# Optimization experiments

Hardware: AMD Instinct MI355X
Metric: run time of the kernel (lower is better)

The kernel has to match this reference:

```python
import jax, jax.numpy as jnp
import numpy as np

HID = 512
EMB = 768
TOP_K = 8
LN_EPS = 1e-5
NORM_EPS = 1e-12


def _mlp_ln(x, W1, b1, W2, b2, g, beta):
    # Linear -> ReLU -> Linear -> LayerNorm
    h = jax.nn.relu(x @ W1 + b1)
    h = h @ W2 + b2
    mu = jnp.mean(h, axis=-1, keepdims=True)
    var = jnp.var(h, axis=-1, keepdims=True)
    return (h - mu) * jax.lax.rsqrt(var + LN_EPS) * g + beta


def _l2norm(x):
    n = jnp.linalg.norm(x, axis=-1, keepdims=True)
    return x / jnp.maximum(n, NORM_EPS)


def setup_inputs() -> dict:
    key = jax.random.key(0)
    ks = jax.random.split(key, 12)
    s_in = 1.0 / np.sqrt(EMB)
    s_h = 1.0 / np.sqrt(HID)
    inp = {
        "query_embeddings": jax.random.normal(ks[0], (64, 32, EMB), jnp.float32),
        "doc_embeddings": jax.random.normal(ks[1], (50000, 16, EMB), jnp.float32),
        "qW1": jax.random.normal(ks[2], (EMB, HID), jnp.float32) * s_in,
        "qb1": jnp.zeros((HID,), jnp.float32),
        "qW2": jax.random.normal(ks[3], (HID, HID), jnp.float32) * s_h,
        "qb2": jnp.zeros((HID,), jnp.float32),
        "qg": jnp.ones((HID,), jnp.float32),
        "qbeta": jnp.zeros((HID,), jnp.float32),
        "dW1": jax.random.normal(ks[4], (EMB, HID), jnp.float32) * s_in,
        "db1": jnp.zeros((HID,), jnp.float32),
        "dW2": jax.random.normal(ks[5], (HID, HID), jnp.float32) * s_h,
        "db2": jnp.zeros((HID,), jnp.float32),
        "dg": jnp.ones((HID,), jnp.float32),
        "dbeta": jnp.zeros((HID,), jnp.float32),
        "pW": jax.random.normal(ks[6], (HID, HID), jnp.float32) * s_h,
        "pb": jnp.zeros((HID,), jnp.float32),
        "temperature": jnp.asarray(1.0, jnp.float32),
    }
    return inp


def reference(query_embeddings, doc_embeddings, qW1, qb1, qW2, qb2, qg, qbeta,
              dW1, db1, dW2, db2, dg, dbeta, pW, pb, temperature):
    # Mean-pool over token dims, encode with MLP+LayerNorm
    q_repr = _mlp_ln(query_embeddings.mean(axis=1), qW1, qb1, qW2, qb2, qg, qbeta)  # [B,H]
    d_repr = _mlp_ln(doc_embeddings.mean(axis=1), dW1, db1, dW2, db2, dg, dbeta)    # [N,H]
    q_norm = _l2norm(q_repr @ pW + pb)
    d_norm = _l2norm(d_repr @ pW + pb)
    scores = (q_norm @ d_norm.T) / temperature  # [B,N]
    top_k_scores, top_k_indices = jax.lax.top_k(scores, TOP_K)  # [B,K]
    retrieved_docs = doc_embeddings[top_k_indices]  # [B,K,doc_len,EMB]
    return top_k_scores, retrieved_docs
```

## Files before the change

kernel.cpp:

```cpp
#include <hip/hip_runtime.h>

#define NQ 64
#define ND 50000
#define QTOK 32
#define DTOK 16
#define EMB 768
#define HID 512

typedef short s16x8 __attribute__((ext_vector_type(8)));
typedef float f32x4 __attribute__((ext_vector_type(4)));

__device__ __forceinline__ unsigned short f2bf(float f) {
    union { float f; unsigned u; } x; x.f = f;
    unsigned r = x.u + 0x7fffu + ((x.u >> 16) & 1u);
    return (unsigned short)(r >> 16);
}
__device__ __forceinline__ float bf2f(unsigned short h) {
    union { unsigned u; float f; } x; x.u = ((unsigned)h) << 16;
    return x.f;
}
__device__ __forceinline__ void packA1(float v, ushort* p) {
    unsigned short hi = f2bf(v);
    unsigned short lo = f2bf(v - bf2f(hi));
    p[0] = hi; p[1] = lo; p[2] = hi;
}
__device__ __forceinline__ void packB1(float v, ushort* p) {
    unsigned short hi = f2bf(v);
    unsigned short lo = f2bf(v - bf2f(hi));
    p[0] = hi; p[1] = hi; p[2] = lo;
}
__device__ __forceinline__ void pack2A(float va, float vb, unsigned& w0, unsigned& w1, unsigned& w2) {
    unsigned ha = f2bf(va); unsigned la = f2bf(va - bf2f((unsigned short)ha));
    unsigned hb = f2bf(vb); unsigned lb = f2bf(vb - bf2f((unsigned short)hb));
    w0 = ha | (la << 16);
    w1 = ha | (hb << 16);
    w2 = lb | (hb << 16);
}

__device__ __forceinline__ void gload_lds16(const void* g, void* l) {
    __builtin_amdgcn_global_load_lds(
        (const __attribute__((address_space(1))) void*)g,
        (__attribute__((address_space(3))) void*)l, 16, 0, 0);
}

__global__ void pool_aug(const float* __restrict__ in, ushort* __restrict__ out, int T) {
    int r = blockIdx.x, t = threadIdx.x;
    const float4* ip = (const float4*)in + (size_t)r * T * (EMB / 4) + t;
    float4 a = make_float4(0.f, 0.f, 0.f, 0.f);
    for (int i = 0; i < T; ++i) {
        float4 v = ip[(size_t)i * (EMB / 4)];
        a.x += v.x; a.y += v.y; a.z += v.z; a.w += v.w;
    }
    const float s = 1.0f / (float)T;
    unsigned w0, w1, w2, w3, w4, w5;
    pack2A(a.x * s, a.y * s, w0, w1, w2);
    pack2A(a.z * s, a.w * s, w3, w4, w5);
    uint2* q = (uint2*)(out + (size_t)r * (3 * EMB) + t * 12);
    q[0] = make_uint2(w0, w1); q[1] = make_uint2(w2, w3); q[2] = make_uint2(w4, w5);
}

__global__ void wconv(const float* __restrict__ W, ushort* __restrict__ Wp, int K) {
    int n = blockIdx.x;
    for (int k = threadIdx.x; k < K; k += blockDim.x) {
        float v = W[(size_t)k * HID + n];
        ushort* p = Wp + (size_t)n * 3 * K + 3 * k;
        packB1(v, p);
    }
}

template <int EPI, int NW>
__global__ __launch_bounds__(NW * 64) void gemmF(const ushort* __restrict__ A,
                                                 const ushort* __restrict__ B,
                                                 const float* __restrict__ bias,
                                                 const float* __restrict__ gamma,
                                                 const float* __restrict__ beta,
                                                 void* __restrict__ out,
                                                 int M, int N_B, int K2, long ldo,
                                                 const float* __restrict__ temp) {
    constexpr int BN = NW * 64;
    constexpr int NTHR = NW * 64;
    __shared__ ushort As[64 * 64];
    __shared__ ushort Bs[BN * 64];
    __shared__ float red[2][NW][64];
    __shared__ float mu_s[64], rs_s[64];
    const int bm = blockIdx.x * 64;
    const int bn = blockIdx.y * BN;
    const int tid = threadIdx.x;
    const int lane = tid & 63;
    const int wc = tid >> 6;
    f32x4 acc[4][4] = {};

    for (int k0 = 0; k0 < K2; k0 += 64) {
        #pragma unroll
        for (int c = 0; c < 512 / NTHR; ++c) {
            int idx = c * NTHR + tid;
            int row = idx >> 3, s = idx & 7;
            int gr = bm + row; if (gr >= M) gr = M - 1;
            int ks = (s ^ (row & 7)) << 3;
            gload_lds16(A + (size_t)gr * K2 + k0 + ks, As + idx * 8);
        }
        #pragma unroll
        for (int c = 0; c < 8; ++c) {
            int idx = c * NTHR + tid;
            int n = idx >> 3, s = idx & 7;
            int gn = bn + n; if (gn >= N_B) gn = N_B - 1;
            int ks = (s ^ (n & 7)) << 3;
            gload_lds16(B + (size_t)gn * K2 + k0 + ks, Bs + idx * 8);
        }
        __syncthreads();

        #pragma unroll
        for (int kk = 0; kk < 2; ++kk) {
            const int sp = kk * 4 + (lane >> 4);
            s16x8 a[4], b[4];
            #pragma unroll
            for (int i = 0; i < 4; ++i) {
                int r = i * 16 + (lane & 15);
                a[i] = *(const s16x8*)(As + r * 64 + ((sp ^ (r & 7)) << 3));
            }
            #pragma unroll
            for (int j = 0; j < 4; ++j) {
                int n = wc * 64 + j * 16 + (lane & 15);
                b[j] = *(const s16x8*)(Bs + n * 64 + ((sp ^ (n & 7)) << 3));
            }
            #pragma unroll
            for (int i = 0; i < 4; ++i)
                #pragma unroll
                for (int j = 0; j < 4; ++j)
                    acc[i][j] = __builtin_amdgcn_mfma_f32_16x16x32_bf16(a[i], b[j], acc[i][j], 0, 0, 0);
        }
        __syncthreads();
    }

    if (EPI == 4) {
        float invT = 1.0f / temp[0];
        #pragma unroll
        for (int j = 0; j < 4; ++j) {
            int gcol = bn + wc * 64 + j * 16 + (lane & 15);
            #pragma unroll
            for (int i = 0; i < 4; ++i)
                #pragma unroll
                for (int r = 0; r < 4; ++r) {
                    int grow = bm + i * 16 + ((lane >> 4) << 2) + r;
                    if (grow < M && gcol < N_B)
                        ((float*)out)[(size_t)grow * ldo + gcol] = acc[i][j][r] * invT;
                }
        }
        return;
    }

    float bv[4];
    #pragma unroll
    for (int j = 0; j < 4; ++j) bv[j] = bias[wc * 64 + j * 16 + (lane & 15)];

    if (EPI == 1 || EPI == 2 || EPI == 3) {
        #pragma unroll
        for (int i = 0; i < 4; ++i)
            #pragma unroll
            for (int r = 0; r < 4; ++r) {
                float ps = 0.f, pq = 0.f;
                #pragma unroll
                for (int j = 0; j < 4; ++j) {
                    float v = acc[i][j][r] + bv[j];
                    ps += v; pq += v * v;
                }
                #pragma unroll
                for (int o = 1; o < 16; o <<= 1) {
                    ps += __shfl_xor(ps, o);
                    pq += __shfl_xor(pq, o);
                }
                if ((lane & 15) == 0) {
                    int rl = i * 16 + ((lane >> 4) << 2) + r;
                    red[0][wc][rl] = ps;
                    red[1][wc][rl] = pq;
                }
            }
        __syncthreads();
        if (tid < 64) {
            float s = 0.f, q = 0.f;
            #pragma unroll
            for (int w = 0; w < NW; ++w) { s += red[0][w][tid]; q += red[1][w][tid]; }
            if (EPI == 1) {
                float mu = s * (1.0f / 512.0f);
                float var = q * (1.0f / 512.0f) - mu * mu;
                mu_s[tid] = mu;
                rs_s[tid] = rsqrtf(var + 1e-5f);
            } else {
                mu_s[tid] = 0.0f;
                rs_s[tid] = 1.0f / fmaxf(sqrtf(q), 1e-12f);
            }
        }
        __syncthreads();
    }

    float gl[4], bt[4];
    if (EPI == 1) {
        #pragma unroll
        for (int j = 0; j < 4; ++j) {
            int c = wc * 64 + j * 16 + (lane & 15);
            gl[j] = gamma[c]; bt[j] = beta[c];
        }
    }

    #pragma unroll
    for (int i = 0; i < 4; ++i)
        #pragma unroll
        for (int r = 0; r < 4; ++r) {
            int rl = i * 16 + ((lane >> 4) << 2) + r;
            int grow = bm + rl;
            if (grow >= M) continue;
            #pragma unroll
            for (int j = 0; j < 4; ++j) {
                int col = wc * 64 + j * 16 + (lane & 15);
                float v = acc[i][j][r] + bv[j];
                if (EPI == 0) v = fmaxf(v, 0.0f);
                else if (EPI == 1) v = (v - mu_s[rl]) * rs_s[rl] * gl[j] + bt[j];
                else v = v * rs_s[rl];
                ushort* op = (ushort*)out + (size_t)grow * (3 * HID) + 3 * col;
                if (EPI == 3) packB1(v, op); else packA1(v, op);
            }
        }
}

__global__ __launch_bounds__(256) void topk_kernel(const float* __restrict__ scores,
                                                   float* __restrict__ out_scores,
                                                   int* __restrict__ out_idx, int N) {
    __shared__ float ls[2048];
    __shared__ int   li[2048];
    const int q   = blockIdx.x;
    const int tid = threadIdx.x;
    const float* row = scores + (size_t)q * N;
    float s[8]; int ix[8];
    #pragma unroll
    for (int i = 0; i < 8; ++i) { s[i] = -1e30f; ix[i] = 0x7fffffff; }
    for (int j = tid; j < N; j += 256) {
        float v = row[j];
        if (v > s[7]) {
            s[7] = v; ix[7] = j;
            #pragma unroll
            for (int t = 7; t > 0; --t) {
                bool sw = (s[t] > s[t-1]) || (s[t] == s[t-1] && ix[t] < ix[t-1]);
                if (sw) {
                    float tv = s[t]; s[t] = s[t-1]; s[t-1] = tv;
                    int   ti = ix[t]; ix[t] = ix[t-1]; ix[t-1] = ti;
                }
            }
        }
    }
    #pragma unroll
    for (int i = 0; i < 8; ++i) { ls[tid * 8 + i] = s[i]; li[tid * 8 + i] = ix[i]; }
    __syncthreads();
    for (int w = 64; w >= 1; w >>= 2) {
        if (tid < w) {
            #pragma unroll
            for (int i = 0; i < 8; ++i) { s[i] = -1e30f; ix[i] = 0x7fffffff; }
            #pragma unroll
            for (int c = 0; c < 32; ++c) {
                float v  = ls[tid * 32 + c];
                int   vi = li[tid * 32 + c];
                bool better = (v > s[7]) || (v == s[7] && vi < ix[7]);
                if (better) {
                    s[7] = v; ix[7] = vi;
                    #pragma unroll
                    for (int t = 7; t > 0; --t) {
                        bool sw = (s[t] > s[t-1]) || (s[t] == s[t-1] && ix[t] < ix[t-1]);
                        if (sw) {
                            float tv = s[t]; s[t] = s[t-1]; s[t-1] = tv;
                            int   ti = ix[t]; ix[t] = ix[t-1]; ix[t-1] = ti;
                        }
                    }
                }
            }
        }
        __syncthreads();
        if (tid < w) {
            #pragma unroll
            for (int i = 0; i < 8; ++i) { ls[tid * 8 + i] = s[i]; li[tid * 8 + i] = ix[i]; }
        }
        __syncthreads();
    }
    if (tid < 8) {
        out_scores[(size_t)q * 8 + tid] = ls[tid];
        out_idx[q * 8 + tid]            = li[tid];
    }
}

__global__ __launch_bounds__(256) void gather_kernel(const float* __restrict__ docs,
                                                     const int* __restrict__ idx,
                                                     float* __restrict__ out) {
    const int b = blockIdx.x;
    const int d = idx[b];
    const float4* src = (const float4*)(docs + (size_t)d * DTOK * EMB);
    float4*       dst = (float4*)(out + (size_t)b * DTOK * EMB);
    for (int i = threadIdx.x; i < DTOK * EMB / 4; i += 256) dst[i] = src[i];
}

extern "C" void kernel_launch(void* const* d_in, const int* in_sizes, int n_in,
                              void* d_out, int out_size, void* d_ws, size_t ws_size,
                              hipStream_t stream) {
    const float* qe   = (const float*)d_in[0];
    const float* de   = (const float*)d_in[1];
    const float* qW1  = (const float*)d_in[2];
    const float* qb1  = (const float*)d_in[3];
    const float* qW2  = (const float*)d_in[4];
    const float* qb2  = (const float*)d_in[5];
    const float* qg   = (const float*)d_in[6];
    const float* qbe  = (const float*)d_in[7];
    const float* dW1  = (const float*)d_in[8];
    const float* db1  = (const float*)d_in[9];
    const float* dW2  = (const float*)d_in[10];
    const float* db2  = (const float*)d_in[11];
    const float* dg   = (const float*)d_in[12];
    const float* dbe  = (const float*)d_in[13];
    const float* pW   = (const float*)d_in[14];
    const float* pb   = (const float*)d_in[15];
    const float* temp = (const float*)d_in[16];

    float* out = (float*)d_out;

    char* w = (char*)d_ws;
    float*  scores = (float*)w;                 w += (size_t)NQ * ND * 4;
    ushort* W1p    = (ushort*)w;                w += (size_t)HID * 3 * EMB * 2;
    ushort* W2p    = (ushort*)w;                w += (size_t)HID * 3 * HID * 2;
    ushort* pWp    = (ushort*)w;                w += (size_t)HID * 3 * HID * 2;
    ushort* QW1p   = (ushort*)w;                w += (size_t)HID * 3 * EMB * 2;
    ushort* QW2p   = (ushort*)w;                w += (size_t)HID * 3 * HID * 2;
    ushort* qpool  = (ushort*)w;                w += (size_t)NQ * 3 * EMB * 2;
    ushort* qh1a   = (ushort*)w;                w += (size_t)NQ * 3 * HID * 2;
    ushort* qlna   = (ushort*)w;                w += (size_t)NQ * 3 * HID * 2;
    ushort* qaug   = (ushort*)w;                w += (size_t)NQ * 3 * HID * 2;
    int*    tidx   = (int*)w;                   w += 4096;
    ushort* pooled = (ushort*)w;                w += (size_t)ND * 3 * EMB * 2;
    ushort* h1a    = (ushort*)w;                w += (size_t)ND * 3 * HID * 2;
    ushort* lna    = pooled;
    ushort* Daug   = h1a;

    const int GMD = (ND + 63) / 64;

    wconv<<<HID, 256, 0, stream>>>(dW1, W1p, EMB);
    wconv<<<HID, 256, 0, stream>>>(dW2, W2p, HID);
    wconv<<<HID, 256, 0, stream>>>(pW,  pWp, HID);
    wconv<<<HID, 256, 0, stream>>>(qW1, QW1p, EMB);
    wconv<<<HID, 256, 0, stream>>>(qW2, QW2p, HID);

    pool_aug<<<NQ, 192, 0, stream>>>(qe, qpool, QTOK);
    gemmF<0, 8><<<dim3(1, 1), 512, 0, stream>>>(qpool, QW1p, qb1, nullptr, nullptr, qh1a,
                                                NQ, HID, 3 * EMB, 0, nullptr);
    gemmF<1, 8><<<dim3(1, 1), 512, 0, stream>>>(qh1a, QW2p, qb2, qg, qbe, qlna,
                                                NQ, HID, 3 * HID, 0, nullptr);
    gemmF<2, 8><<<dim3(1, 1), 512, 0, stream>>>(qlna, pWp, pb, nullptr, nullptr, qaug,
                                                NQ, HID, 3 * HID, 0, nullptr);

    pool_aug<<<ND, 192, 0, stream>>>(de, pooled, DTOK);
    gemmF<0, 8><<<dim3(GMD, 1), 512, 0, stream>>>(pooled, W1p, db1, nullptr, nullptr, h1a,
                                                  ND, HID, 3 * EMB, 0, nullptr);
    gemmF<1, 8><<<dim3(GMD, 1), 512, 0, stream>>>(h1a, W2p, db2, dg, dbe, lna,
                                                  ND, HID, 3 * HID, 0, nullptr);
    gemmF<3, 8><<<dim3(GMD, 1), 512, 0, stream>>>(lna, pWp, pb, nullptr, nullptr, Daug,
                                                  ND, HID, 3 * HID, 0, nullptr);

    gemmF<4, 4><<<dim3(1, (ND + 255) / 256), 256, 0, stream>>>(qaug, Daug, nullptr, nullptr, nullptr,
                                                               scores, NQ, ND, 3 * HID, (long)ND, temp);

    topk_kernel<<<NQ, 256, 0, stream>>>(scores, out, tidx, ND);
    gather_kernel<<<NQ * 8, 256, 0, stream>>>(de, tidx, out + NQ * 8);
}
```

Baseline: 1.594 ms.

## Retile doc GEMMs to 128x256 with XCD-aware mapping and split LN/L2 epilogues

```diff
diff --git a/kernel.cpp b/kernel.cpp
--- a/kernel.cpp
+++ b/kernel.cpp
@@ -35,6 +35,13 @@
     w0 = ha | (la << 16);
     w1 = ha | (hb << 16);
     w2 = lb | (hb << 16);
+}
+__device__ __forceinline__ void pack2B(float va, float vb, unsigned& w0, unsigned& w1, unsigned& w2) {
+    unsigned ha = f2bf(va); unsigned la = f2bf(va - bf2f((unsigned short)ha));
+    unsigned hb = f2bf(vb); unsigned lb = f2bf(vb - bf2f((unsigned short)hb));
+    w0 = ha | (ha << 16);
+    w1 = la | (hb << 16);
+    w2 = hb | (lb << 16);
 }
 
 __device__ __forceinline__ void gload_lds16(const void* g, void* l) {
@@ -68,44 +75,196 @@
     }
 }
 
-template <int EPI, int NW>
-__global__ __launch_bounds__(NW * 64) void gemmF(const ushort* __restrict__ A,
-                                                 const ushort* __restrict__ B,
-                                                 const float* __restrict__ bias,
-                                                 const float* __restrict__ gamma,
-                                                 const float* __restrict__ beta,
-                                                 void* __restrict__ out,
-                                                 int M, int N_B, int K2, long ldo,
-                                                 const float* __restrict__ temp) {
-    constexpr int BN = NW * 64;
-    constexpr int NTHR = NW * 64;
+template <int MODE>
+__global__ __launch_bounds__(512) void mfma_gemm2(const ushort* __restrict__ A,
+                                                  const ushort* __restrict__ B,
+                                                  const float* __restrict__ bias,
+                                                  void* __restrict__ out,
+                                                  int M, int K2) {
+    __shared__ ushort As[128 * 64];
+    __shared__ ushort Bs[256 * 64];
+    const int nwg = gridDim.x;
+    const int d   = blockIdx.x;
+    const int qq  = nwg >> 3, rr = nwg & 7;
+    const int x   = d & 7, slot = d >> 3;
+    const int base = (x < rr) ? x * (qq + 1) : rr * (qq + 1) + (x - rr) * qq;
+    const int g   = base + slot;
+    const int bm  = (g >> 1) * 128;
+    const int bn  = (g & 1) * 256;
+    const int tid = threadIdx.x;
+    const int lane = tid & 63;
+    const int wave = tid >> 6;
+    const int wr = wave >> 2;
+    const int wc = wave & 3;
+    f32x4 acc[4][4] = {};
+
+    for (int k0 = 0; k0 < K2; k0 += 64) {
+        #pragma unroll
+        for (int c = 0; c < 2; ++c) {
+            int idx = c * 512 + tid;
+            int row = idx >> 3, s = idx & 7;
+            int gr = bm + row; if (gr >= M) gr = M - 1;
+            int ks = (s ^ (row & 7)) << 3;
+            gload_lds16(A + (size_t)gr * K2 + k0 + ks, As + idx * 8);
+        }
+        #pragma unroll
+        for (int c = 0; c < 4; ++c) {
+            int idx = c * 512 + tid;
+            int n = idx >> 3, s = idx & 7;
+            int ks = (s ^ (n & 7)) << 3;
+            gload_lds16(B + (size_t)(bn + n) * K2 + k0 + ks, Bs + idx * 8);
+        }
+        __syncthreads();
+
+        #pragma unroll
+        for (int kk = 0; kk < 2; ++kk) {
+            const int sp = kk * 4 + (lane >> 4);
+            s16x8 a[4], b[4];
+            #pragma unroll
+            for (int i = 0; i < 4; ++i) {
+                int r = wr * 64 + i * 16 + (lane & 15);
+                a[i] = *(const s16x8*)(As + r * 64 + ((sp ^ (r & 7)) << 3));
+            }
+            #pragma unroll
+            for (int j = 0; j < 4; ++j) {
+                int n = wc * 64 + j * 16 + (lane & 15);
+                b[j] = *(const s16x8*)(Bs + n * 64 + ((sp ^ (n & 7)) << 3));
+            }
+            #pragma unroll
+            for (int i = 0; i < 4; ++i)
+                #pragma unroll
+                for (int j = 0; j < 4; ++j)
+                    acc[i][j] = __builtin_amdgcn_mfma_f32_16x16x32_bf16(a[i], b[j], acc[i][j], 0, 0, 0);
+        }
+        __syncthreads();
+    }
+
+    #pragma unroll
+    for (int j = 0; j < 4; ++j) {
+        int col = bn + wc * 64 + j * 16 + (lane & 15);
+        float bv = bias[col];
+        #pragma unroll
+        for (int i = 0; i < 4; ++i) {
+            #pragma unroll
+            for (int r = 0; r < 4; ++r) {
+                int grow = bm + wr * 64 + i * 16 + ((lane >> 4) << 2) + r;
+                if (grow >= M) continue;
+                float v = acc[i][j][r] + bv;
+                if (MODE == 1) {
+                    v = fmaxf(v, 0.0f);
+                    ushort* op = (ushort*)out + (size_t)grow * (3 * HID) + 3 * col;
+                    packA1(v, op);
+                } else {
+                    ((float*)out)[(size_t)grow * HID + col] = v;
+                }
+            }
+        }
+    }
+}
+
+__global__ __launch_bounds__(512) void mfma_scores(const ushort* __restrict__ A,
+                                                   const ushort* __restrict__ B,
+                                                   float* __restrict__ out,
+                                                   int M, int N_B, int K2, long ldo,
+                                                   const float* __restrict__ temp) {
+    __shared__ ushort As[128 * 64];
+    __shared__ ushort Bs[256 * 64];
+    const int bm = blockIdx.x * 128;
+    const int bn = blockIdx.y * 256;
+    const int tid = threadIdx.x;
+    const int lane = tid & 63;
+    const int wave = tid >> 6;
+    const int wr = wave >> 2;
+    const int wc = wave & 3;
+    f32x4 acc[4][4] = {};
+
+    for (int k0 = 0; k0 < K2; k0 += 64) {
+        #pragma unroll
+        for (int c = 0; c < 2; ++c) {
+            int idx = c * 512 + tid;
+            int row = idx >> 3, s = idx & 7;
+            int gr = bm + row; if (gr >= M) gr = M - 1;
+            int ks = (s ^ (row & 7)) << 3;
+            gload_lds16(A + (size_t)gr * K2 + k0 + ks, As + idx * 8);
+        }
+        #pragma unroll
+        for (int c = 0; c < 4; ++c) {
+            int idx = c * 512 + tid;
+            int n = idx >> 3, s = idx & 7;
+            int gn = bn + n; if (gn >= N_B) gn = N_B - 1;
+            int ks = (s ^ (n & 7)) << 3;
+            gload_lds16(B + (size_t)gn * K2 + k0 + ks, Bs + idx * 8);
+        }
+        __syncthreads();
+
+        #pragma unroll
+        for (int kk = 0; kk < 2; ++kk) {
+            const int sp = kk * 4 + (lane >> 4);
+            s16x8 a[4], b[4];
+            #pragma unroll
+            for (int i = 0; i < 4; ++i) {
+                int r = wr * 64 + i * 16 + (lane & 15);
+                a[i] = *(const s16x8*)(As + r * 64 + ((sp ^ (r & 7)) << 3));
+            }
+            #pragma unroll
+            for (int j = 0; j < 4; ++j) {
+                int n = wc * 64 + j * 16 + (lane & 15);
+                b[j] = *(const s16x8*)(Bs + n * 64 + ((sp ^ (n & 7)) << 3));
+            }
+            #pragma unroll
+            for (int i = 0; i < 4; ++i)
+                #pragma unroll
+                for (int j = 0; j < 4; ++j)
+                    acc[i][j] = __builtin_amdgcn_mfma_f32_16x16x32_bf16(a[i], b[j], acc[i][j], 0, 0, 0);
+        }
+        __syncthreads();
+    }
+
+    float invT = 1.0f / temp[0];
+    #pragma unroll
+    for (int j = 0; j < 4; ++j) {
+        int gcol = bn + wc * 64 + j * 16 + (lane & 15);
+        #pragma unroll
+        for (int i = 0; i < 4; ++i)
+            #pragma unroll
+            for (int r = 0; r < 4; ++r) {
+                int grow = bm + wr * 64 + i * 16 + ((lane >> 4) << 2) + r;
+                if (grow < M && gcol < N_B)
+                    out[(size_t)grow * ldo + gcol] = acc[i][j][r] * invT;
+            }
+    }
+}
+
+template <int EPI>
+__global__ __launch_bounds__(512) void gemmF(const ushort* __restrict__ A,
+                                             const ushort* __restrict__ B,
+                                             const float* __restrict__ bias,
+                                             const float* __restrict__ gamma,
+                                             const float* __restrict__ beta,
+                                             ushort* __restrict__ out,
+                                             int M, int K2) {
     __shared__ ushort As[64 * 64];
-    __shared__ ushort Bs[BN * 64];
-    __shared__ float red[2][NW][64];
+    __shared__ ushort Bs[512 * 64];
+    __shared__ float red[2][8][64];
     __shared__ float mu_s[64], rs_s[64];
-    const int bm = blockIdx.x * 64;
-    const int bn = blockIdx.y * BN;
     const int tid = threadIdx.x;
     const int lane = tid & 63;
     const int wc = tid >> 6;
     f32x4 acc[4][4] = {};
 
     for (int k0 = 0; k0 < K2; k0 += 64) {
-        #pragma unroll
-        for (int c = 0; c < 512 / NTHR; ++c) {
-            int idx = c * NTHR + tid;
-            int row = idx >> 3, s = idx & 7;
-            int gr = bm + row; if (gr >= M) gr = M - 1;
+        {
+            int row = tid >> 3, s = tid & 7;
+            int gr = row; if (gr >= M) gr = M - 1;
             int ks = (s ^ (row & 7)) << 3;
-            gload_lds16(A + (size_t)gr * K2 + k0 + ks, As + idx * 8);
+            gload_lds16(A + (size_t)gr * K2 + k0 + ks, As + tid * 8);
         }
         #pragma unroll
         for (int c = 0; c < 8; ++c) {
-            int idx = c * NTHR + tid;
+            int idx = c * 512 + tid;
             int n = idx >> 3, s = idx & 7;
-            int gn = bn + n; if (gn >= N_B) gn = N_B - 1;
             int ks = (s ^ (n & 7)) << 3;
-            gload_lds16(B + (size_t)gn * K2 + k0 + ks, Bs + idx * 8);
+            gload_lds16(B + (size_t)n * K2 + k0 + ks, Bs + idx * 8);
         }
         __syncthreads();
 
@@ -132,28 +291,11 @@
         __syncthreads();
     }
 
-    if (EPI == 4) {
-        float invT = 1.0f / temp[0];
-        #pragma unroll
-        for (int j = 0; j < 4; ++j) {
-            int gcol = bn + wc * 64 + j * 16 + (lane & 15);
-            #pragma unroll
-            for (int i = 0; i < 4; ++i)
-                #pragma unroll
-                for (int r = 0; r < 4; ++r) {
-                    int grow = bm + i * 16 + ((lane >> 4) << 2) + r;
-                    if (grow < M && gcol < N_B)
-                        ((float*)out)[(size_t)grow * ldo + gcol] = acc[i][j][r] * invT;
-                }
-        }
-        return;
-    }
-
     float bv[4];
     #pragma unroll
     for (int j = 0; j < 4; ++j) bv[j] = bias[wc * 64 + j * 16 + (lane & 15)];
 
-    if (EPI == 1 || EPI == 2 || EPI == 3) {
+    if (EPI == 1 || EPI == 2) {
         #pragma unroll
         for (int i = 0; i < 4; ++i)
             #pragma unroll
@@ -179,7 +321,7 @@
         if (tid < 64) {
             float s = 0.f, q = 0.f;
             #pragma unroll
-            for (int w = 0; w < NW; ++w) { s += red[0][w][tid]; q += red[1][w][tid]; }
+            for (int w = 0; w < 8; ++w) { s += red[0][w][tid]; q += red[1][w][tid]; }
             if (EPI == 1) {
                 float mu = s * (1.0f / 512.0f);
                 float var = q * (1.0f / 512.0f) - mu * mu;
@@ -207,8 +349,7 @@
         #pragma unroll
         for (int r = 0; r < 4; ++r) {
             int rl = i * 16 + ((lane >> 4) << 2) + r;
-            int grow = bm + rl;
-            if (grow >= M) continue;
+            if (rl >= M) continue;
             #pragma unroll
             for (int j = 0; j < 4; ++j) {
                 int col = wc * 64 + j * 16 + (lane & 15);
@@ -216,10 +357,71 @@
                 if (EPI == 0) v = fmaxf(v, 0.0f);
                 else if (EPI == 1) v = (v - mu_s[rl]) * rs_s[rl] * gl[j] + bt[j];
                 else v = v * rs_s[rl];
-                ushort* op = (ushort*)out + (size_t)grow * (3 * HID) + 3 * col;
-                if (EPI == 3) packB1(v, op); else packA1(v, op);
-            }
-        }
+                packA1(v, out + (size_t)rl * (3 * HID) + 3 * col);
+            }
+        }
+}
+
+__global__ __launch_bounds__(256) void ln_aug(const float* __restrict__ x,
+                                              const float* __restrict__ g,
+                                              const float* __restrict__ be,
+                                              ushort* __restrict__ out, int M) {
+    int wv = threadIdx.x >> 6, lane = threadIdx.x & 63;
+    int row = blockIdx.x * 4 + wv;
+    if (row >= M) return;
+    const float4* p = (const float4*)(x + (size_t)row * HID);
+    float4 a = p[lane * 2], b = p[lane * 2 + 1];
+    float s  = a.x + a.y + a.z + a.w + b.x + b.y + b.z + b.w;
+    float sq = a.x*a.x + a.y*a.y + a.z*a.z + a.w*a.w
+             + b.x*b.x + b.y*b.y + b.z*b.z + b.w*b.w;
+    #pragma unroll
+    for (int o = 32; o > 0; o >>= 1) { s += __shfl_xor(s, o); sq += __shfl_xor(sq, o); }
+    float mu  = s * (1.0f / HID);
+    float var = sq * (1.0f / HID) - mu * mu;
+    float r   = rsqrtf(var + 1e-5f);
+    const float4* gp = (const float4*)g;
+    const float4* bp = (const float4*)be;
+    float4 g0 = gp[lane * 2], g1 = gp[lane * 2 + 1];
+    float4 b0 = bp[lane * 2], b1 = bp[lane * 2 + 1];
+    float v0 = (a.x - mu) * r * g0.x + b0.x, v1 = (a.y - mu) * r * g0.y + b0.y;
+    float v2 = (a.z - mu) * r * g0.z + b0.z, v3 = (a.w - mu) * r * g0.w + b0.w;
+    float v4 = (b.x - mu) * r * g1.x + b1.x, v5 = (b.y - mu) * r * g1.y + b1.y;
+    float v6 = (b.z - mu) * r * g1.z + b1.z, v7 = (b.w - mu) * r * g1.w + b1.w;
+    unsigned w[12];
+    pack2A(v0, v1, w[0], w[1], w[2]);
+    pack2A(v2, v3, w[3], w[4], w[5]);
+    pack2A(v4, v5, w[6], w[7], w[8]);
+    pack2A(v6, v7, w[9], w[10], w[11]);
+    uint4* q = (uint4*)(out + (size_t)row * (3 * HID) + lane * 24);
+    q[0] = make_uint4(w[0], w[1], w[2], w[3]);
+    q[1] = make_uint4(w[4], w[5], w[6], w[7]);
+    q[2] = make_uint4(w[8], w[9], w[10], w[11]);
+}
+
+__global__ __launch_bounds__(256) void l2_augB(const float* __restrict__ x,
+                                               ushort* __restrict__ out, int M) {
+    int wv = threadIdx.x >> 6, lane = threadIdx.x & 63;
+    int row = blockIdx.x * 4 + wv;
+    if (row >= M) return;
+    const float4* p = (const float4*)(x + (size_t)row * HID);
+    float4 a = p[lane * 2], b = p[lane * 2 + 1];
+    float sq = a.x*a.x + a.y*a.y + a.z*a.z + a.w*a.w
+             + b.x*b.x + b.y*b.y + b.z*b.z + b.w*b.w;
+    #pragma unroll
+    for (int o = 32; o > 0; o >>= 1) sq += __shfl_xor(sq, o);
+    float n = sqrtf(sq);
+    float r = 1.0f / fmaxf(n, 1e-12f);
+    float v0 = a.x*r, v1 = a.y*r, v2 = a.z*r, v3 = a.w*r;
+    float v4 = b.x*r, v5 = b.y*r, v6 = b.z*r, v7 = b.w*r;
+    unsigned w[12];
+    pack2B(v0, v1, w[0], w[1], w[2]);
+    pack2B(v2, v3, w[3], w[4], w[5]);
+    pack2B(v4, v5, w[6], w[7], w[8]);
+    pack2B(v6, v7, w[9], w[10], w[11]);
+    uint4* q = (uint4*)(out + (size_t)row * (3 * HID) + lane * 24);
+    q[0] = make_uint4(w[0], w[1], w[2], w[3]);
+    q[1] = make_uint4(w[4], w[5], w[6], w[7]);
+    q[2] = make_uint4(w[8], w[9], w[10], w[11]);
 }
 
 __global__ __launch_bounds__(256) void topk_kernel(const float* __restrict__ scores,
@@ -332,10 +534,13 @@
     int*    tidx   = (int*)w;                   w += 4096;
     ushort* pooled = (ushort*)w;                w += (size_t)ND * 3 * EMB * 2;
     ushort* h1a    = (ushort*)w;                w += (size_t)ND * 3 * HID * 2;
+    float*  h2     = (float*)w;                 w += (size_t)ND * HID * 4;
     ushort* lna    = pooled;
+    float*  pproj  = h2;
     ushort* Daug   = h1a;
 
-    const int GMD = (ND + 63) / 64;
+    const int NPAN = (ND + 127) / 128;
+    const int NWG  = NPAN * 2;
 
     wconv<<<HID, 256, 0, stream>>>(dW1, W1p, EMB);
     wconv<<<HID, 256, 0, stream>>>(dW2, W2p, HID);
@@ -344,23 +549,19 @@
     wconv<<<HID, 256, 0, stream>>>(qW2, QW2p, HID);
 
     pool_aug<<<NQ, 192, 0, stream>>>(qe, qpool, QTOK);
-    gemmF<0, 8><<<dim3(1, 1), 512, 0, stream>>>(qpool, QW1p, qb1, nullptr, nullptr, qh1a,
-                                                NQ, HID, 3 * EMB, 0, nullptr);
-    gemmF<1, 8><<<dim3(1, 1), 512, 0, stream>>>(qh1a, QW2p, qb2, qg, qbe, qlna,
-                                                NQ, HID, 3 * HID, 0, nullptr);
-    gemmF<2, 8><<<dim3(1, 1), 512, 0, stream>>>(qlna, pWp, pb, nullptr, nullptr, qaug,
-                                                NQ, HID, 3 * HID, 0, nullptr);
+    gemmF<0><<<1, 512, 0, stream>>>(qpool, QW1p, qb1, nullptr, nullptr, qh1a, NQ, 3 * EMB);
+    gemmF<1><<<1, 512, 0, stream>>>(qh1a, QW2p, qb2, qg, qbe, qlna, NQ, 3 * HID);
+    gemmF<2><<<1, 512, 0, stream>>>(qlna, pWp, pb, nullptr, nullptr, qaug, NQ, 3 * HID);
 
     pool_aug<<<ND, 192, 0, stream>>>(de, pooled, DTOK);
-    gemmF<0, 8><<<dim3(GMD, 1), 512, 0, stream>>>(pooled, W1p, db1, nullptr, nullptr, h1a,
-                                                  ND, HID, 3 * EMB, 0, nullptr);
-    gemmF<1, 8><<<dim3(GMD, 1), 512, 0, stream>>>(h1a, W2p, db2, dg, dbe, lna,
-                                                  ND, HID, 3 * HID, 0, nullptr);
-    gemmF<3, 8><<<dim3(GMD, 1), 512, 0, stream>>>(lna, pWp, pb, nullptr, nullptr, Daug,
-                                                  ND, HID, 3 * HID, 0, nullptr);
-
-    gemmF<4, 4><<<dim3(1, (ND + 255) / 256), 256, 0, stream>>>(qaug, Daug, nullptr, nullptr, nullptr,
-                                                               scores, NQ, ND, 3 * HID, (long)ND, temp);
+    mfma_gemm2<1><<<NWG, 512, 0, stream>>>(pooled, W1p, db1, h1a, ND, 3 * EMB);
+    mfma_gemm2<0><<<NWG, 512, 0, stream>>>(h1a, W2p, db2, h2, ND, 3 * HID);
+    ln_aug<<<(ND + 3) / 4, 256, 0, stream>>>(h2, dg, dbe, lna, ND);
+    mfma_gemm2<0><<<NWG, 512, 0, stream>>>(lna, pWp, pb, pproj, ND, 3 * HID);
+    l2_augB<<<(ND + 3) / 4, 256, 0, stream>>>(pproj, Daug, ND);
+
+    mfma_scores<<<dim3(1, (ND + 255) / 256), 512, 0, stream>>>(qaug, Daug, scores,
+                                                               NQ, ND, 3 * HID, (long)ND, temp);
 
     topk_kernel<<<NQ, 256, 0, stream>>>(scores, out, tidx, ND);
     gather_kernel<<<NQ * 8, 256, 0, stream>>>(de, tidx, out + NQ * 8);
```

New measurement: 1.604 ms. About the same (+0.6%).
